# Kernel optimization log

Hardware: AMD Instinct MI355X
Metric: run time of the kernel (lower is better)

Reference implementation:

```python
import jax, jax.numpy as jnp
import numpy as np

D_MODEL = 1024
N_HEADS = 16
D_FF = 4096
EPS = 1e-5


def setup_inputs() -> dict:
    key = jax.random.key(0)
    ks = jax.random.split(key, 16)
    s = 1.0 / np.sqrt(D_MODEL)
    x = jax.random.normal(ks[0], (4, 2048, D_MODEL), dtype=jnp.float32)
    Wq = jax.random.normal(ks[1], (D_MODEL, D_MODEL), jnp.float32) * s
    bq = jnp.zeros((D_MODEL,), jnp.float32)
    Wk = jax.random.normal(ks[2], (D_MODEL, D_MODEL), jnp.float32) * s
    bk = jnp.zeros((D_MODEL,), jnp.float32)
    Wv = jax.random.normal(ks[3], (D_MODEL, D_MODEL), jnp.float32) * s
    bv = jnp.zeros((D_MODEL,), jnp.float32)
    Wo = jax.random.normal(ks[4], (D_MODEL, D_MODEL), jnp.float32) * s
    bo = jnp.zeros((D_MODEL,), jnp.float32)
    W1 = jax.random.normal(ks[5], (D_MODEL, D_FF), jnp.float32) * s
    b1 = jnp.zeros((D_FF,), jnp.float32)
    W2 = jax.random.normal(ks[6], (D_FF, D_MODEL), jnp.float32) * (1.0 / np.sqrt(D_FF))
    b2 = jnp.zeros((D_MODEL,), jnp.float32)
    g1 = jnp.ones((D_MODEL,), jnp.float32)
    beta1 = jnp.zeros((D_MODEL,), jnp.float32)
    g2 = jnp.ones((D_MODEL,), jnp.float32)
    beta2 = jnp.zeros((D_MODEL,), jnp.float32)
    return {"x": x, "Wq": Wq, "bq": bq, "Wk": Wk, "bk": bk, "Wv": Wv, "bv": bv,
            "Wo": Wo, "bo": bo, "W1": W1, "b1": b1, "W2": W2, "b2": b2,
            "g1": g1, "beta1": beta1, "g2": g2, "beta2": beta2}


def _layernorm(x, g, b):
    mu = jnp.mean(x, axis=-1, keepdims=True)
    var = jnp.mean(jnp.square(x - mu), axis=-1, keepdims=True)
    return (x - mu) * jax.lax.rsqrt(var + EPS) * g + b


def reference(x, Wq, bq, Wk, bk, Wv, bv, Wo, bo, W1, b1, W2, b2, g1, beta1, g2, beta2):
    B, S, D = x.shape
    H, dk = N_HEADS, D // N_HEADS
    # QKV projections -> [B, H, S, dk]
    q = (x @ Wq + bq).reshape(B, S, H, dk).transpose(0, 2, 1, 3)
    k = (x @ Wk + bk).reshape(B, S, H, dk).transpose(0, 2, 1, 3)
    v = (x @ Wv + bv).reshape(B, S, H, dk).transpose(0, 2, 1, 3)
    scores = jnp.einsum('bhqd,bhkd->bhqk', q, k) / np.sqrt(dk)  # [B,H,S,S]
    attn = jax.nn.softmax(scores, axis=-1)
    out = jnp.einsum('bhqk,bhkd->bhqd', attn, v)
    out = out.transpose(0, 2, 1, 3).reshape(B, S, D) @ Wo + bo
    x2 = _layernorm(x + out, g1, beta1)
    ff = jax.nn.relu(x2 @ W1 + b1) @ W2 + b2
    return _layernorm(x2 + ff, g2, beta2)
```

## Files before the change

kernel.cpp:

```cpp
#include <hip/hip_runtime.h>
#include <math.h>
#include <stdint.h>


#define D_MODEL 1024
#define N_HEADS 16
#define DKH     64
#define D_FF    4096
#define BATCH   4
#define SEQ     2048
#define NTOK    (BATCH * SEQ)
#define LN_EPS  1e-5f
#define QKV_LD  3072
#define QSCALE  0.18033688011112042f

typedef unsigned short u16;
typedef __attribute__((ext_vector_type(8))) short bf16x8;
typedef __attribute__((ext_vector_type(4))) float f32x4;
typedef __attribute__((ext_vector_type(16))) float f32x16;

__device__ __forceinline__ u16 f2bf(float f) {
    union { float f; uint32_t u; } c; c.f = f;
    return (u16)((c.u + 0x7FFFu + ((c.u >> 16) & 1u)) >> 16);
}
__device__ __forceinline__ float bf2f(u16 h) {
    union { uint32_t u; float f; } c; c.u = ((uint32_t)h) << 16;
    return c.f;
}

__device__ __forceinline__ void gload16(const u16* g, u16* lds) {
    __builtin_amdgcn_global_load_lds(
        (const __attribute__((address_space(1))) uint32_t*)g,
        (__attribute__((address_space(3))) uint32_t*)(uintptr_t)lds,
        16, 0, 0);
}

__device__ __forceinline__ void store_out(float* p, float v) { *p = v; }
__device__ __forceinline__ void store_out(u16* p, float v)   { *p = f2bf(v); }

template <int MODE, typename OutT>
__global__ __launch_bounds__(512) void gemm_pipe_kernel(
    const u16* __restrict__ A, const u16* __restrict__ Bt,
    const float* __restrict__ bias, const float* __restrict__ bias2,
    const float* __restrict__ bias3, OutT* __restrict__ C,
    int M, int N, int K)
{
    __shared__ u16 lds[3 * 8192 + 2 * 16384];

    const int tid  = threadIdx.x;
    const int wave = tid >> 6;
    const int lane = tid & 63;
    const int lo   = lane & 15;
    const int hi   = lane >> 4;
    const int wr   = wave >> 2;
    const int wc   = wave & 3;
    const int m0   = blockIdx.y << 7;
    const int n0   = blockIdx.x << 8;
    const int NT   = K >> 6;

    const int srow = lane >> 3;
    const int schk = (lane & 7) ^ srow;
    const u16* AgS = A  + (size_t)(m0 + wave * 16 + srow) * K + schk * 8;
    const u16* BgS = Bt + (size_t)(n0 + wave * 32 + srow) * K + schk * 8;
    u16* AdS = lds + wave * 1024;
    u16* BdS = lds + 24576 + wave * 2048;

    auto stageA = [&](int kt, int buf) {
        const u16* g = AgS + kt * 64;
        u16* d = AdS + buf * 8192;
#pragma unroll
        for (int q = 0; q < 2; ++q)
            gload16(g + (size_t)q * 8 * K, d + q * 512);
    };
    auto stageB = [&](int kt, int buf) {
        const u16* g = BgS + kt * 64;
        u16* d = BdS + buf * 16384;
#pragma unroll
        for (int q = 0; q < 4; ++q)
            gload16(g + (size_t)q * 8 * K, d + q * 512);
    };

    f32x4 acc[4][4];
#pragma unroll
    for (int i = 0; i < 4; ++i)
#pragma unroll
        for (int j = 0; j < 4; ++j)
#pragma unroll
            for (int r = 0; r < 4; ++r) acc[i][j][r] = 0.f;

    stageA(0, 0);
    stageB(0, 0);
    stageA(1, 1);
    __builtin_amdgcn_sched_barrier(0);
    asm volatile("s_waitcnt vmcnt(2)" ::: "memory");
    __builtin_amdgcn_s_barrier();
    __builtin_amdgcn_sched_barrier(0);

    for (int t = 0; t < NT; ++t) {
        int tb = t + 1; if (tb >= NT) tb = 0;
        int ta = t + 2; if (ta >= NT) ta -= NT;
        stageB(tb, (t + 1) & 1);
        stageA(ta, (t + 2) % 3);

        const u16* Ab = lds + (t % 3) * 8192;
        const u16* Bb = lds + 24576 + (t & 1) * 16384;
#pragma unroll
        for (int ks = 0; ks < 2; ++ks) {
            bf16x8 a[4], b[4];
#pragma unroll
            for (int i = 0; i < 4; ++i) {
                const int ar = wr * 64 + i * 16 + lo;
                a[i] = *(const bf16x8*)&Ab[ar * 64 + (((ks * 4 + hi) ^ (ar & 7)) << 3)];
                const int br = wc * 64 + i * 16 + lo;
                b[i] = *(const bf16x8*)&Bb[br * 64 + (((ks * 4 + hi) ^ (br & 7)) << 3)];
            }
            __builtin_amdgcn_s_setprio(1);
#pragma unroll
            for (int i = 0; i < 4; ++i)
#pragma unroll
                for (int j = 0; j < 4; ++j)
                    acc[i][j] = __builtin_amdgcn_mfma_f32_16x16x32_bf16(
                                    a[i], b[j], acc[i][j], 0, 0, 0);
            __builtin_amdgcn_s_setprio(0);
        }
        __builtin_amdgcn_sched_barrier(0);
        asm volatile("s_waitcnt vmcnt(2)" ::: "memory");
        __builtin_amdgcn_s_barrier();
        __builtin_amdgcn_sched_barrier(0);
    }

    const int crow0 = m0 + wr * 64 + hi * 4;
    const int ccol0 = n0 + wc * 64 + lo;
#pragma unroll
    for (int j = 0; j < 4; ++j) {
        const int col = ccol0 + j * 16;
        float bj;
        float sc = 1.0f;
        if (MODE == 2) {
            bj = (col < 1024) ? bias[col]
               : (col < 2048) ? bias2[col - 1024] : bias3[col - 2048];
            if (col < 1024) sc = QSCALE;
        } else {
            bj = bias[col];
        }
#pragma unroll
        for (int i = 0; i < 4; ++i)
#pragma unroll
            for (int r = 0; r < 4; ++r) {
                float v = acc[i][j][r] + bj;
                if (MODE == 1) v = fmaxf(v, 0.f);
                if (MODE == 2) v *= sc;
                store_out(&C[(size_t)(crow0 + i * 16 + r) * N + col], v);
            }
    }
}

__global__ __launch_bounds__(256, 3) void attn_mfma_kernel(
    const u16* __restrict__ QKV, u16* __restrict__ O)
{
    __shared__ u16 Klds[64 * 64];
    __shared__ u16 Vlds[64 * 64];

    const int tid  = threadIdx.x;
    const int wave = tid >> 6;
    const int lane = tid & 63;
    const int l31  = lane & 31;
    const int hi5  = lane >> 5;
    const int b    = blockIdx.x >> 4;
    const int h    = blockIdx.x & 15;
    const int q0   = blockIdx.y * 128 + wave * 32;
    const size_t rowb = (size_t)b * SEQ * QKV_LD + (size_t)h * DKH;
    const u16* Qg = QKV + rowb;
    const u16* Kg = QKV + rowb + 1024;
    const u16* Vg = QKV + rowb + 2048;

    bf16x8 qf[4];
#pragma unroll
    for (int f = 0; f < 4; ++f)
        qf[f] = *(const bf16x8*)&Qg[(size_t)(q0 + l31) * QKV_LD + 16 * f + 8 * hi5];

    f32x16 oacc[2];
#pragma unroll
    for (int g = 0; g < 2; ++g)
#pragma unroll
        for (int r = 0; r < 16; ++r) oacc[g][r] = 0.f;
    float mrun = -1e30f, lrun = 0.f;

    const int krow = wave * 8 + (lane >> 3);
    const int kchk = ((lane & 7) ^ (lane >> 3)) << 3;
    u16* kdst = Klds + wave * 512;

    const int vdk0 = (tid & 15) * 4;
    const int vkv  = (tid >> 4) * 4;
    const int vchk = vkv >> 3;
    const int vsub = vkv & 7;

    for (int kv0 = 0; kv0 < SEQ; kv0 += 64) {
        __syncthreads();
        gload16(Kg + (size_t)(kv0 + krow) * QKV_LD + kchk,      kdst);
        gload16(Kg + (size_t)(kv0 + krow + 32) * QKV_LD + kchk, kdst + 32 * 64);
        alignas(8) u16 e[4][4];
#pragma unroll
        for (int i = 0; i < 4; ++i)
            *(uint2*)e[i] = *(const uint2*)&Vg[(size_t)(kv0 + vkv + i) * QKV_LD + vdk0];
#pragma unroll
        for (int j = 0; j < 4; ++j) {
            alignas(8) u16 w4[4] = { e[0][j], e[1][j], e[2][j], e[3][j] };
            const int row = vdk0 + j;
            *(uint2*)&Vlds[row * 64 + ((vchk ^ (row & 7)) << 3) + vsub] = *(const uint2*)w4;
        }
        __syncthreads();

        f32x16 s0, s1;
#pragma unroll
        for (int r = 0; r < 16; ++r) { s0[r] = 0.f; s1[r] = 0.f; }
#pragma unroll
        for (int f = 0; f < 4; ++f) {
            const int rc = ((2 * f + hi5) ^ (l31 & 7)) << 3;
            const bf16x8 ka = *(const bf16x8*)&Klds[l31 * 64 + rc];
            const bf16x8 kb = *(const bf16x8*)&Klds[(32 + l31) * 64 + rc];
            s0 = __builtin_amdgcn_mfma_f32_32x32x16_bf16(ka, qf[f], s0, 0, 0, 0);
            s1 = __builtin_amdgcn_mfma_f32_32x32x16_bf16(kb, qf[f], s1, 0, 0, 0);
        }

        float tm = s0[0];
#pragma unroll
        for (int r = 1; r < 16; ++r) tm = fmaxf(tm, s0[r]);
#pragma unroll
        for (int r = 0; r < 16; ++r) tm = fmaxf(tm, s1[r]);
        tm = fmaxf(tm, __shfl_xor(tm, 32, 64));
        if (__any(tm > mrun + 8.0f)) {
            const float mnew = fmaxf(mrun, tm);
            const float corr = exp2f(mrun - mnew);
            lrun *= corr;
#pragma unroll
            for (int g = 0; g < 2; ++g)
#pragma unroll
                for (int r = 0; r < 16; ++r) oacc[g][r] *= corr;
            mrun = mnew;
        }
        float ls = 0.f;
#pragma unroll
        for (int r = 0; r < 16; ++r) { s0[r] = exp2f(s0[r] - mrun); ls += s0[r]; }
#pragma unroll
        for (int r = 0; r < 16; ++r) { s1[r] = exp2f(s1[r] - mrun); ls += s1[r]; }
        lrun += ls;

        auto mkfrag = [&](float a0, float a1, float a2, float a3,
                          float a4, float a5, float a6, float a7) -> bf16x8 {
            uint32_t A, B, C, D;
            asm("v_cvt_pk_bf16_f32 %0, %1, %2" : "=v"(A) : "v"(a0), "v"(a1));
            asm("v_cvt_pk_bf16_f32 %0, %1, %2" : "=v"(C) : "v"(a2), "v"(a3));
            asm("v_cvt_pk_bf16_f32 %0, %1, %2" : "=v"(B) : "v"(a4), "v"(a5));
            asm("v_cvt_pk_bf16_f32 %0, %1, %2" : "=v"(D) : "v"(a6), "v"(a7));
            asm volatile("v_permlane32_swap_b32 %0, %1" : "+v"(A), "+v"(B));
            asm volatile("v_permlane32_swap_b32 %0, %1" : "+v"(C), "+v"(D));
            union { uint32_t w[4]; bf16x8 v; } u;
            u.w[0] = A; u.w[1] = C; u.w[2] = B; u.w[3] = D;
            return u.v;
        };
        bf16x8 pb0 = mkfrag(s0[0], s0[1], s0[2],  s0[3],  s0[4],  s0[5],  s0[6],  s0[7]);
        bf16x8 pb1 = mkfrag(s0[8], s0[9], s0[10], s0[11], s0[12], s0[13], s0[14], s0[15]);
        bf16x8 pb2 = mkfrag(s1[0], s1[1], s1[2],  s1[3],  s1[4],  s1[5],  s1[6],  s1[7]);
        bf16x8 pb3 = mkfrag(s1[8], s1[9], s1[10], s1[11], s1[12], s1[13], s1[14], s1[15]);

#pragma unroll
        for (int f = 0; f < 4; ++f) {
            const bf16x8 pf = (f == 0) ? pb0 : (f == 1) ? pb1 : (f == 2) ? pb2 : pb3;
            const int rc = ((2 * f + hi5) ^ (l31 & 7)) << 3;
            const bf16x8 va = *(const bf16x8*)&Vlds[l31 * 64 + rc];
            const bf16x8 vb = *(const bf16x8*)&Vlds[(32 + l31) * 64 + rc];
            oacc[0] = __builtin_amdgcn_mfma_f32_32x32x16_bf16(va, pf, oacc[0], 0, 0, 0);
            oacc[1] = __builtin_amdgcn_mfma_f32_32x32x16_bf16(vb, pf, oacc[1], 0, 0, 0);
        }
    }

    lrun += __shfl_xor(lrun, 32, 64);
    const float inv = 1.0f / lrun;
    u16* Orow = O + (size_t)b * SEQ * D_MODEL + (size_t)(q0 + l31) * D_MODEL + h * DKH;
#pragma unroll
    for (int g = 0; g < 2; ++g)
#pragma unroll
        for (int rp = 0; rp < 8; ++rp) {
            const int r = rp * 2;
            const float v0 = oacc[g][r] * inv;
            const float v1 = oacc[g][r + 1] * inv;
            uint32_t pk;
            asm("v_cvt_pk_bf16_f32 %0, %1, %2" : "=v"(pk) : "v"(v0), "v"(v1));
            const int d = 32 * g + (r & 3) + 8 * (r >> 2) + 4 * hi5;
            *(uint32_t*)&Orow[d] = pk;
        }
}

__global__ __launch_bounds__(256) void transpose_w_kernel(
    const float* __restrict__ W, u16* __restrict__ Wt, int K, int N)
{
    __shared__ float t[32][33];
    const int n0 = blockIdx.x << 5;
    const int k0 = blockIdx.y << 5;
    const int tx = threadIdx.x & 31;
    const int ty = threadIdx.x >> 5;
#pragma unroll
    for (int i = 0; i < 4; ++i)
        t[ty + i * 8][tx] = W[(size_t)(k0 + ty + i * 8) * N + n0 + tx];
    __syncthreads();
#pragma unroll
    for (int i = 0; i < 4; ++i)
        Wt[(size_t)(n0 + ty + i * 8) * K + k0 + tx] = f2bf(t[tx][ty + i * 8]);
}

__global__ __launch_bounds__(256) void cvt_kernel(
    const float* __restrict__ src, u16* __restrict__ dst)
{
    const size_t i = ((size_t)blockIdx.x * 256 + threadIdx.x) * 8;
    const float4 a = *(const float4*)&src[i];
    const float4 b = *(const float4*)&src[i + 4];
    alignas(16) u16 e[8] = { f2bf(a.x), f2bf(a.y), f2bf(a.z), f2bf(a.w),
                             f2bf(b.x), f2bf(b.y), f2bf(b.z), f2bf(b.w) };
    *(int4*)&dst[i] = *(const int4*)e;
}

__device__ __forceinline__ float4 ld4(const float* p) { return *(const float4*)p; }
__device__ __forceinline__ float4 ld4(const u16* p) {
    alignas(8) u16 e[4];
    *(uint2*)e = *(const uint2*)p;
    return make_float4(bf2f(e[0]), bf2f(e[1]), bf2f(e[2]), bf2f(e[3]));
}
__device__ __forceinline__ void st4(float* p, float4 v) { *(float4*)p = v; }
__device__ __forceinline__ void st4(u16* p, float4 v) {
    alignas(8) u16 e[4] = { f2bf(v.x), f2bf(v.y), f2bf(v.z), f2bf(v.w) };
    *(uint2*)p = *(const uint2*)e;
}

template <typename XT, typename YT, typename OT>
__global__ __launch_bounds__(256) void add_ln_kernel(
    const XT* __restrict__ X, const YT* __restrict__ Y,
    const float* __restrict__ gamma, const float* __restrict__ beta,
    OT* __restrict__ Out)
{
    const int row = blockIdx.x;
    const int i0  = threadIdx.x << 2;
    const float4 xv = ld4(X + (size_t)row * D_MODEL + i0);
    const float4 yv = ld4(Y + (size_t)row * D_MODEL + i0);
    const float4 v  = make_float4(xv.x + yv.x, xv.y + yv.y, xv.z + yv.z, xv.w + yv.w);

    float s1 = v.x + v.y + v.z + v.w;
    float s2 = v.x * v.x + v.y * v.y + v.z * v.z + v.w * v.w;
#pragma unroll
    for (int off = 32; off > 0; off >>= 1) {
        s1 += __shfl_xor(s1, off, 64);
        s2 += __shfl_xor(s2, off, 64);
    }
    __shared__ float red[8];
    const int wid = threadIdx.x >> 6;
    if ((threadIdx.x & 63) == 0) { red[wid] = s1; red[wid + 4] = s2; }
    __syncthreads();
    s1 = red[0] + red[1] + red[2] + red[3];
    s2 = red[4] + red[5] + red[6] + red[7];

    const float mu   = s1 * (1.0f / D_MODEL);
    const float var  = s2 * (1.0f / D_MODEL) - mu * mu;
    const float rstd = rsqrtf(var + LN_EPS);

    const float4 g  = *(const float4*)(gamma + i0);
    const float4 bb = *(const float4*)(beta + i0);
    float4 ov;
    ov.x = (v.x - mu) * rstd * g.x + bb.x;
    ov.y = (v.y - mu) * rstd * g.y + bb.y;
    ov.z = (v.z - mu) * rstd * g.z + bb.z;
    ov.w = (v.w - mu) * rstd * g.w + bb.w;
    st4(Out + (size_t)row * D_MODEL + i0, ov);
}

extern "C" void kernel_launch(void* const* d_in, const int* in_sizes, int n_in,
                              void* d_out, int out_size, void* d_ws, size_t ws_size,
                              hipStream_t stream)
{
    const float* x     = (const float*)d_in[0];
    const float* Wq    = (const float*)d_in[1];
    const float* bq    = (const float*)d_in[2];
    const float* Wk    = (const float*)d_in[3];
    const float* bk    = (const float*)d_in[4];
    const float* Wv    = (const float*)d_in[5];
    const float* bv    = (const float*)d_in[6];
    const float* Wo    = (const float*)d_in[7];
    const float* bo    = (const float*)d_in[8];
    const float* W1    = (const float*)d_in[9];
    const float* b1    = (const float*)d_in[10];
    const float* W2    = (const float*)d_in[11];
    const float* b2    = (const float*)d_in[12];
    const float* g1    = (const float*)d_in[13];
    const float* beta1 = (const float*)d_in[14];
    const float* g2    = (const float*)d_in[15];
    const float* beta2 = (const float*)d_in[16];
    float* out = (float*)d_out;

    const size_t TOKD = (size_t)NTOK * D_MODEL;
    u16* xb    = (u16*)d_ws;
    u16* wqkvT = xb + TOKD;
    u16* woT   = wqkvT + (size_t)3 * D_MODEL * D_MODEL;
    u16* w1T   = woT + (size_t)D_MODEL * D_MODEL;
    u16* w2T   = w1T + (size_t)D_MODEL * D_FF;
    u16* qkv   = w2T + (size_t)D_FF * D_MODEL;
    u16* ctx   = qkv + (size_t)NTOK * QKV_LD;
    u16* y1    = ctx + TOKD;
    u16* x2    = y1;
    u16* h1    = qkv;

    const dim3 blk(256);
    const dim3 blk5(512);

    cvt_kernel<<<dim3(TOKD / 2048), blk, 0, stream>>>(x, xb);
    transpose_w_kernel<<<dim3(D_MODEL / 32, D_MODEL / 32), blk, 0, stream>>>(Wq, wqkvT, D_MODEL, D_MODEL);
    transpose_w_kernel<<<dim3(D_MODEL / 32, D_MODEL / 32), blk, 0, stream>>>(Wk, wqkvT + (size_t)D_MODEL * D_MODEL, D_MODEL, D_MODEL);
    transpose_w_kernel<<<dim3(D_MODEL / 32, D_MODEL / 32), blk, 0, stream>>>(Wv, wqkvT + (size_t)2 * D_MODEL * D_MODEL, D_MODEL, D_MODEL);
    transpose_w_kernel<<<dim3(D_MODEL / 32, D_MODEL / 32), blk, 0, stream>>>(Wo, woT, D_MODEL, D_MODEL);
    transpose_w_kernel<<<dim3(D_FF / 32,    D_MODEL / 32), blk, 0, stream>>>(W1, w1T, D_MODEL, D_FF);
    transpose_w_kernel<<<dim3(D_MODEL / 32, D_FF / 32),    blk, 0, stream>>>(W2, w2T, D_FF, D_MODEL);

    gemm_pipe_kernel<2, u16><<<dim3(QKV_LD / 256, NTOK / 128), blk5, 0, stream>>>(
        xb, wqkvT, bq, bk, bv, qkv, NTOK, QKV_LD, D_MODEL);

    attn_mfma_kernel<<<dim3(BATCH * N_HEADS, SEQ / 128), blk, 0, stream>>>(qkv, ctx);

    gemm_pipe_kernel<0, u16><<<dim3(D_MODEL / 256, NTOK / 128), blk5, 0, stream>>>(
        ctx, woT, bo, bo, bo, y1, NTOK, D_MODEL, D_MODEL);

    add_ln_kernel<float, u16, u16><<<dim3(NTOK), blk, 0, stream>>>(x, y1, g1, beta1, x2);

    gemm_pipe_kernel<1, u16><<<dim3(D_FF / 256, NTOK / 128), blk5, 0, stream>>>(
        x2, w1T, b1, b1, b1, h1, NTOK, D_FF, D_MODEL);
    gemm_pipe_kernel<0, float><<<dim3(D_MODEL / 256, NTOK / 128), blk5, 0, stream>>>(
        h1, w2T, b2, b2, b2, out, NTOK, D_MODEL, D_FF);

    add_ln_kernel<u16, float, float><<<dim3(NTOK), blk, 0, stream>>>(x2, out, g2, beta2, out);

    (void)in_sizes; (void)n_in; (void)out_size; (void)ws_size;
}
```

Before: 414.2 us.

## Double-buffer attention K/V tiles, tree reductions, and XCD-aware GEMM block remap

The attention kernel now double-buffers its K and V tiles in LDS. It prefetches the next tile's K (async global-to-LDS) and V (into registers) while computing the current tile, which leaves one barrier per iteration instead of two. The row max and sum reductions become tree reductions to shorten the dependency chains, and the occupancy hint rises from 3 to 4 blocks. The GEMM kernel remaps block IDs so consecutive tiles land on the same XCD chiplet, aiming for better L2 reuse. In exchange, attention uses twice the LDS and may come under register pressure from the held V values at higher occupancy.

After: 407.7 us. About the same (-1.6%).

```diff
diff --git a/kernel.cpp b/kernel.cpp
--- a/kernel.cpp
+++ b/kernel.cpp
@@ -54,9 +54,14 @@
     const int hi   = lane >> 4;
     const int wr   = wave >> 2;
     const int wc   = wave & 3;
-    const int m0   = blockIdx.y << 7;
-    const int n0   = blockIdx.x << 8;
-    const int NT   = K >> 6;
+
+    const int gx  = gridDim.x;
+    const int nwg = gx * gridDim.y;
+    int bid = blockIdx.y * gx + blockIdx.x;
+    bid = (bid & 7) * (nwg >> 3) + (bid >> 3);
+    const int m0 = (bid / gx) << 7;
+    const int n0 = (bid % gx) << 8;
+    const int NT = K >> 6;
 
     const int srow = lane >> 3;
     const int schk = (lane & 7) ^ srow;
@@ -155,11 +160,11 @@
     }
 }
 
-__global__ __launch_bounds__(256, 3) void attn_mfma_kernel(
+__global__ __launch_bounds__(256, 4) void attn_mfma_kernel(
     const u16* __restrict__ QKV, u16* __restrict__ O)
 {
-    __shared__ u16 Klds[64 * 64];
-    __shared__ u16 Vlds[64 * 64];
+    __shared__ u16 Klds[2][64 * 64];
+    __shared__ u16 Vlds[2][64 * 64];
 
     const int tid  = threadIdx.x;
     const int wave = tid >> 6;
@@ -188,28 +193,46 @@
 
     const int krow = wave * 8 + (lane >> 3);
     const int kchk = ((lane & 7) ^ (lane >> 3)) << 3;
-    u16* kdst = Klds + wave * 512;
 
     const int vdk0 = (tid & 15) * 4;
     const int vkv  = (tid >> 4) * 4;
     const int vchk = vkv >> 3;
     const int vsub = vkv & 7;
 
-    for (int kv0 = 0; kv0 < SEQ; kv0 += 64) {
-        __syncthreads();
+    alignas(8) u16 e[4][4];
+
+    auto stageK = [&](int kv0, int buf) {
+        u16* kdst = &Klds[buf][wave * 512];
         gload16(Kg + (size_t)(kv0 + krow) * QKV_LD + kchk,      kdst);
         gload16(Kg + (size_t)(kv0 + krow + 32) * QKV_LD + kchk, kdst + 32 * 64);
-        alignas(8) u16 e[4][4];
+    };
+    auto loadV = [&](int kv0) {
 #pragma unroll
         for (int i = 0; i < 4; ++i)
             *(uint2*)e[i] = *(const uint2*)&Vg[(size_t)(kv0 + vkv + i) * QKV_LD + vdk0];
+    };
+    auto writeV = [&](int buf) {
 #pragma unroll
         for (int j = 0; j < 4; ++j) {
             alignas(8) u16 w4[4] = { e[0][j], e[1][j], e[2][j], e[3][j] };
             const int row = vdk0 + j;
-            *(uint2*)&Vlds[row * 64 + ((vchk ^ (row & 7)) << 3) + vsub] = *(const uint2*)w4;
-        }
-        __syncthreads();
+            *(uint2*)&Vlds[buf][row * 64 + ((vchk ^ (row & 7)) << 3) + vsub] =
+                *(const uint2*)w4;
+        }
+    };
+
+    stageK(0, 0);
+    loadV(0);
+    writeV(0);
+    __syncthreads();
+
+    constexpr int NTILES = SEQ / 64;
+    for (int t = 0; t < NTILES; ++t) {
+        const int cur = t & 1, nxt = cur ^ 1;
+        if (t + 1 < NTILES) {
+            stageK((t + 1) * 64, nxt);
+            loadV((t + 1) * 64);
+        }
 
         f32x16 s0, s1;
 #pragma unroll
@@ -217,18 +240,20 @@
 #pragma unroll
         for (int f = 0; f < 4; ++f) {
             const int rc = ((2 * f + hi5) ^ (l31 & 7)) << 3;
-            const bf16x8 ka = *(const bf16x8*)&Klds[l31 * 64 + rc];
-            const bf16x8 kb = *(const bf16x8*)&Klds[(32 + l31) * 64 + rc];
+            const bf16x8 ka = *(const bf16x8*)&Klds[cur][l31 * 64 + rc];
+            const bf16x8 kb = *(const bf16x8*)&Klds[cur][(32 + l31) * 64 + rc];
             s0 = __builtin_amdgcn_mfma_f32_32x32x16_bf16(ka, qf[f], s0, 0, 0, 0);
             s1 = __builtin_amdgcn_mfma_f32_32x32x16_bf16(kb, qf[f], s1, 0, 0, 0);
         }
 
-        float tm = s0[0];
-#pragma unroll
-        for (int r = 1; r < 16; ++r) tm = fmaxf(tm, s0[r]);
-#pragma unroll
-        for (int r = 0; r < 16; ++r) tm = fmaxf(tm, s1[r]);
-        tm = fmaxf(tm, __shfl_xor(tm, 32, 64));
+        float mx[16];
+#pragma unroll
+        for (int r = 0; r < 16; ++r) mx[r] = fmaxf(s0[r], s1[r]);
+#pragma unroll
+        for (int off = 8; off >= 1; off >>= 1)
+#pragma unroll
+            for (int r = 0; r < off; ++r) mx[r] = fmaxf(mx[r], mx[r + off]);
+        float tm = fmaxf(mx[0], __shfl_xor(mx[0], 32, 64));
         if (__any(tm > mrun + 8.0f)) {
             const float mnew = fmaxf(mrun, tm);
             const float corr = exp2f(mrun - mnew);
@@ -239,12 +264,20 @@
                 for (int r = 0; r < 16; ++r) oacc[g][r] *= corr;
             mrun = mnew;
         }
-        float ls = 0.f;
-#pragma unroll
-        for (int r = 0; r < 16; ++r) { s0[r] = exp2f(s0[r] - mrun); ls += s0[r]; }
-#pragma unroll
-        for (int r = 0; r < 16; ++r) { s1[r] = exp2f(s1[r] - mrun); ls += s1[r]; }
-        lrun += ls;
+        float sm[16];
+#pragma unroll
+        for (int r = 0; r < 16; ++r) {
+            s0[r] = exp2f(s0[r] - mrun);
+            s1[r] = exp2f(s1[r] - mrun);
+            sm[r] = s0[r] + s1[r];
+        }
+#pragma unroll
+        for (int off = 8; off >= 1; off >>= 1)
+#pragma unroll
+            for (int r = 0; r < off; ++r) sm[r] += sm[r + off];
+        lrun += sm[0];
+
+        if (t + 1 < NTILES) writeV(nxt);
 
         auto mkfrag = [&](float a0, float a1, float a2, float a3,
                           float a4, float a5, float a6, float a7) -> bf16x8 {
@@ -268,11 +301,12 @@
         for (int f = 0; f < 4; ++f) {
             const bf16x8 pf = (f == 0) ? pb0 : (f == 1) ? pb1 : (f == 2) ? pb2 : pb3;
             const int rc = ((2 * f + hi5) ^ (l31 & 7)) << 3;
-            const bf16x8 va = *(const bf16x8*)&Vlds[l31 * 64 + rc];
-            const bf16x8 vb = *(const bf16x8*)&Vlds[(32 + l31) * 64 + rc];
+            const bf16x8 va = *(const bf16x8*)&Vlds[cur][l31 * 64 + rc];
+            const bf16x8 vb = *(const bf16x8*)&Vlds[cur][(32 + l31) * 64 + rc];
             oacc[0] = __builtin_amdgcn_mfma_f32_32x32x16_bf16(va, pf, oacc[0], 0, 0, 0);
             oacc[1] = __builtin_amdgcn_mfma_f32_32x32x16_bf16(vb, pf, oacc[1], 0, 0, 0);
         }
+        __syncthreads();
     }
 
     lrun += __shfl_xor(lrun, 32, 64);
```
